# Kernel optimization log

Hardware: AMD Instinct MI355X
Metric: run time of the kernel (lower is better)

The kernel has to match this reference:

```python
import jax, jax.numpy as jnp
import numpy as np

B, T, E, H = 2, 4096, 1024, 16
SEGS = (256, 512, 1024, 2048, 4096)
DILS = (1, 2, 4, 8, 16)
NEG = -1e8  # torchscale uses -1e8 for uncovered / masked lse entries


def setup_inputs() -> dict:
    key = jax.random.key(0)
    ks = jax.random.split(key, 5)
    sc = 0.02
    zb = jnp.zeros((E,), jnp.float32)
    return {
        "x": jax.random.normal(ks[0], (B, T, E), jnp.float32),
        "wq": jax.random.normal(ks[1], (E, E), jnp.float32) * sc,
        "bq": zb,
        "wk": jax.random.normal(ks[2], (E, E), jnp.float32) * sc,
        "bk": zb,
        "wv": jax.random.normal(ks[3], (E, E), jnp.float32) * sc,
        "bv": zb,
        "wo": jax.random.normal(ks[4], (E, E), jnp.float32) * sc,
        "bo": zb,
    }


def _scale_attn(q, k, v, w, r):
    # One LongNet scale: segment length w, dilation ratio r.
    # Head group g = head // (H//r) attends to in-segment positions p with p % r == g
    # (torchscale dense_to_sparse diagonal over (r1, r2)).
    Bq, Tq, Hq, d = q.shape
    n, s, hp = Tq // w, w // r, Hq // r  # segments, sparse length, heads per group

    def gather(x):
        # [B,T,H,d] -> segments [B,n,w,H,d]; split w=(s,r1) (p=l*r+r1) and H=(r2,hp);
        # keep diagonal r1 == r2.
        x = x.reshape(Bq, n, s, r, r, hp, d)
        x = jnp.diagonal(x, axis1=3, axis2=4)          # [B,n,s,hp,d,r]
        return jnp.moveaxis(x, -1, 3).reshape(Bq, n, s, Hq, d)

    qs, ks_, vs = gather(q), gather(k), gather(v)
    scores = jnp.einsum('bnqhd,bnkhd->bnhqk', qs, ks_)
    mask = jnp.tril(jnp.ones((s, s), dtype=bool))       # causal within sparse segment
    scores = jnp.where(mask, scores, NEG)
    lse = jax.scipy.special.logsumexp(scores, axis=-1)  # [B,n,h,q]
    out = jnp.einsum('bnhqk,bnkhd->bnqhd', jax.nn.softmax(scores, axis=-1), vs)

    # Scatter back to dense positions (sparse_to_dense): uncovered -> out 0, lse -1e8.
    eye = jnp.eye(r, dtype=out.dtype)
    out_g = out.reshape(Bq, n, s, r, hp, d)                               # heads as (g, hp)
    dense = jnp.einsum('bnsghd,pg->bnspghd', out_g, eye).reshape(Bq, Tq, Hq, d)
    lse_g = jnp.transpose(lse, (0, 1, 3, 2)).reshape(Bq, n, s, r, hp)     # [B,n,s,g,hp]
    lse_d = jnp.where(eye[:, :, None] > 0, lse_g[:, :, :, None, :, :], NEG)
    return dense, lse_d.reshape(Bq, Tq, Hq)


def reference(x, wq, bq, wk, bk, wv, bv, wo, bo):
    d = E // H
    q = (x @ wq + bq).reshape(B, T, H, d) * (d ** -0.5)
    k = (x @ wk + bk).reshape(B, T, H, d)
    v = (x @ wv + bv).reshape(B, T, H, d)
    outs, lses = [], []
    for w_, r_ in zip(SEGS, DILS):
        o, l = _scale_attn(q, k, v, w_, r_)
        outs.append(o)
        lses.append(l)
    # Merge scales with softmax over per-scale log-sum-exp (dense-attention equivalence).
    wgt = jax.nn.softmax(jnp.stack(lses), axis=0)[..., None]  # [S,B,T,H,1]
    y = jnp.sum(jnp.stack(outs) * wgt, axis=0).reshape(B, T, E)
    return y @ wo + bo
```

## Files before the change

### kernel.cpp

```cpp
#include <hip/hip_runtime.h>
#include <hip/hip_bf16.h>

typedef __bf16 bf16_t;
typedef __bf16 bf16x8 __attribute__((ext_vector_type(8)));
typedef __bf16 bf16x4 __attribute__((ext_vector_type(4)));
typedef float f32x4 __attribute__((ext_vector_type(4)));
typedef int vint4 __attribute__((ext_vector_type(4)));

#define AS1 __attribute__((address_space(1)))
#define AS3 __attribute__((address_space(3)))

constexpr int B_ = 2, T_ = 4096, E_ = 1024, H_ = 16;
constexpr int M_ = B_ * T_;

__device__ constexpr size_t OB_OFF[5]  = {0, 8388608, 12582912, 14680064, 15728640};
__device__ constexpr size_t LSE_OFF[5] = {0, 131072, 196608, 229376, 245760};
constexpr size_t OB_TOTAL  = 16252928;
constexpr size_t LSE_TOTAL = 253952;

__global__ __launch_bounds__(256) void cvt_f32_bf16(const float* __restrict__ in,
                                                    bf16_t* __restrict__ out) {
  int i = (blockIdx.x * 256 + threadIdx.x) * 4;
  const float4 v = *(const float4*)(in + i);
  bf16x4 o;
  o[0] = (bf16_t)v.x; o[1] = (bf16_t)v.y; o[2] = (bf16_t)v.z; o[3] = (bf16_t)v.w;
  *(bf16x4*)(out + i) = o;
}

__global__ __launch_bounds__(256) void cvt_transpose_w(
    const float* __restrict__ w0, const float* __restrict__ w1,
    const float* __restrict__ w2, const float* __restrict__ w3,
    bf16_t* __restrict__ o0, bf16_t* __restrict__ o1,
    bf16_t* __restrict__ o2, bf16_t* __restrict__ o3) {
  __shared__ float tile[32][33];
  const float* src; bf16_t* dst;
  switch (blockIdx.z) {
    case 0: src = w0; dst = o0; break;
    case 1: src = w1; dst = o1; break;
    case 2: src = w2; dst = o2; break;
    default: src = w3; dst = o3; break;
  }
  const int n0 = blockIdx.x * 32, k0 = blockIdx.y * 32;
  const int tx = threadIdx.x & 31, ty = threadIdx.x >> 5;
#pragma unroll
  for (int i = 0; i < 32; i += 8)
    tile[ty + i][tx] = src[(size_t)(k0 + ty + i) * E_ + n0 + tx];
  __syncthreads();
#pragma unroll
  for (int i = 0; i < 32; i += 8)
    dst[(size_t)(n0 + ty + i) * E_ + k0 + tx] = (bf16_t)tile[tx][ty + i];
}

template <bool OUT_BF16, bool QKV>
__global__ __launch_bounds__(256, 4) void gemm_bt(
    const bf16_t* __restrict__ A, const bf16_t* __restrict__ BT,
    const float* __restrict__ bias0, const float* __restrict__ bias1,
    const float* __restrict__ bias2, void* __restrict__ Cout, float qscale) {
  constexpr int K = E_;
  __shared__ bf16_t As[128 * 64];
  __shared__ bf16_t Bs[128 * 64];
  const int tid = threadIdx.x;
  const int lane = tid & 63;
  const int wave = tid >> 6;
  const int wm = wave >> 1, wn = wave & 1;
  const int lc = lane & 15, lg = lane >> 4;
  const int bm = blockIdx.x;
  int bn = blockIdx.y;

  const float* bias = bias0;
  float scale = 1.0f;
  void* outp = Cout;
  const bf16_t* Bt = BT;
  if (QKV) {
    const int which = bn >> 3;
    bn &= 7;
    bias = (which == 0) ? bias0 : (which == 1) ? bias1 : bias2;
    scale = (which == 0) ? qscale : 1.0f;
    outp = (void*)((bf16_t*)Cout + (size_t)which * M_ * E_);
    Bt += (size_t)which * E_ * E_;
  }

  f32x4 acc[4][4] = {};

  const int lrow = tid >> 3;
  const int schunk = (tid & 7) ^ (lrow & 7);
  const bf16_t* Ag = A + (size_t)(bm * 128 + lrow) * K + schunk * 8;
  const bf16_t* Bg = Bt + (size_t)(bn * 128 + lrow) * K + schunk * 8;

  const int sl0 = ((0 * 4 + lg) ^ (lc & 7)) * 8;
  const int sl1 = ((1 * 4 + lg) ^ (lc & 7)) * 8;

  for (int k0 = 0; k0 < K; k0 += 64) {
    __syncthreads();
#pragma unroll
    for (int p = 0; p < 4; ++p) {
      __builtin_amdgcn_global_load_lds(
          (const AS1 void*)(Ag + (size_t)(p * 32) * K + k0),
          (AS3 void*)(As + p * 2048 + tid * 8), 16, 0, 0);
      __builtin_amdgcn_global_load_lds(
          (const AS1 void*)(Bg + (size_t)(p * 32) * K + k0),
          (AS3 void*)(Bs + p * 2048 + tid * 8), 16, 0, 0);
    }
    __syncthreads();
#pragma unroll
    for (int kk = 0; kk < 2; ++kk) {
      const int sl = kk ? sl1 : sl0;
      bf16x8 af[4], bfr[4];
#pragma unroll
      for (int i = 0; i < 4; ++i) {
        af[i]  = *(const bf16x8*)&As[(wm * 64 + i * 16 + lc) * 64 + sl];
        bfr[i] = *(const bf16x8*)&Bs[(wn * 64 + i * 16 + lc) * 64 + sl];
      }
#pragma unroll
      for (int i = 0; i < 4; ++i)
#pragma unroll
        for (int j = 0; j < 4; ++j)
          acc[i][j] = __builtin_amdgcn_mfma_f32_16x16x32_bf16(af[i], bfr[j], acc[i][j], 0, 0, 0);
    }
  }

#pragma unroll
  for (int i = 0; i < 4; ++i) {
    const int row = bm * 128 + wm * 64 + i * 16 + lg * 4;
#pragma unroll
    for (int j = 0; j < 4; ++j) {
      const int col = bn * 128 + wn * 64 + j * 16 + lc;
      const float bv = bias[col];
#pragma unroll
      for (int rg = 0; rg < 4; ++rg) {
        const float v = (acc[i][j][rg] + bv) * scale;
        if (OUT_BF16)
          ((bf16_t*)outp)[(size_t)(row + rg) * E_ + col] = (bf16_t)v;
        else
          ((float*)outp)[(size_t)(row + rg) * E_ + col] = v;
      }
    }
  }
}

template <bool S0>
__global__ __launch_bounds__(512, 4) void attn_inst(
    const bf16_t* __restrict__ Q, const bf16_t* __restrict__ K,
    const bf16_t* __restrict__ V, bf16_t* __restrict__ Ob,
    float* __restrict__ Lse, bf16_t* __restrict__ Y) {
  __shared__ alignas(16) bf16_t Ks[256][72];
  __shared__ alignas(16) bf16_t Vt[64][264];
  __shared__ alignas(16) bf16_t Pw[8][16][40];

  const int bid = blockIdx.x;
  int s, ibase;
  if (S0) { s = 0; ibase = 0; }
  else if (bid < 256) { s = 1; ibase = 0; }
  else if (bid < 384) { s = 2; ibase = 256; }
  else if (bid < 448) { s = 3; ibase = 384; }
  else                { s = 4; ibase = 448; }
  const int inst = bid - ibase;
  const int h = inst & 15;
  const int nseg_log = 4 - s;
  const int seg = (inst >> 4) & ((1 << nseg_log) - 1);
  const int b = inst >> (4 + nseg_log);
  const int g = h >> (4 - s);

  const int t = threadIdx.x;
  const int lane = t & 63;
  const int wv = t >> 6;
  const int lc = lane & 15;
  const int lg = lane >> 4;

  {
    const int row = t >> 1, ch = (t & 1) * 32;
    const int tk = ((seg * 256 + row) << s) + g;
    const size_t off = ((size_t)b * T_ + tk) * E_ + h * 64 + ch;
    const bf16_t* Kg = K + off;
    const bf16_t* Vg = V + off;
#pragma unroll
    for (int j = 0; j < 4; ++j)
      *(bf16x8*)&Ks[row][ch + j * 8] = *(const bf16x8*)(Kg + j * 8);
#pragma unroll
    for (int j = 0; j < 4; ++j) {
      bf16x8 va = *(const bf16x8*)(Vg + j * 8);
#pragma unroll
      for (int e = 0; e < 8; ++e) Vt[ch + j * 8 + e][row] = va[e];
    }
  }
  __syncthreads();

  const size_t rowbase = (size_t)(b * H_ + h) * (T_ >> s) + seg * 256;

#pragma unroll
  for (int sel = 0; sel < 2; ++sel) {
    const int tile = sel ? (15 - wv) : wv;
    const int q = tile * 16 + lc;

    const int tq = ((seg * 256 + q) << s) + g;
    const bf16_t* Qg = Q + ((size_t)b * T_ + tq) * E_ + h * 64 + lg * 8;
    bf16x8 qfrag0 = *(const bf16x8*)(Qg);
    bf16x8 qfrag1 = *(const bf16x8*)(Qg + 32);

    float m = -INFINITY, Z = 0.0f;
    f32x4 Oa[4] = {};

    const int nkb = tile / 4 + 1;
    const int diag = tile / 4;
    for (int kb = 0; kb < nkb; ++kb) {
      f32x4 sacc[4] = {};
      __builtin_amdgcn_s_setprio(1);
#pragma unroll
      for (int kt = 0; kt < 4; ++kt) {
        bf16x8 kf0 = *(const bf16x8*)&Ks[kb * 64 + kt * 16 + lc][lg * 8];
        bf16x8 kf1 = *(const bf16x8*)&Ks[kb * 64 + kt * 16 + lc][32 + lg * 8];
        sacc[kt] = __builtin_amdgcn_mfma_f32_16x16x32_bf16(kf0, qfrag0, sacc[kt], 0, 0, 0);
        sacc[kt] = __builtin_amdgcn_mfma_f32_16x16x32_bf16(kf1, qfrag1, sacc[kt], 0, 0, 0);
      }
      __builtin_amdgcn_s_setprio(0);
      if (kb == diag) {
#pragma unroll
        for (int kt = 0; kt < 4; ++kt)
#pragma unroll
          for (int rg = 0; rg < 4; ++rg)
            if (kb * 64 + kt * 16 + lg * 4 + rg > q) sacc[kt][rg] = -1e30f;
      }
      float pm = -1e30f;
#pragma unroll
      for (int kt = 0; kt < 4; ++kt) {
        pm = fmaxf(pm, fmaxf(fmaxf(sacc[kt][0], sacc[kt][1]),
                             fmaxf(sacc[kt][2], sacc[kt][3])));
      }
      pm = fmaxf(pm, __shfl_xor(pm, 16));
      pm = fmaxf(pm, __shfl_xor(pm, 32));
      if (!__all(pm - m <= 11.5f)) {
        const float nm = fmaxf(m, pm);
        const float crr = __builtin_amdgcn_exp2f(m - nm);
        Z *= crr;
#pragma unroll
        for (int dt = 0; dt < 4; ++dt)
#pragma unroll
          for (int rg = 0; rg < 4; ++rg) Oa[dt][rg] *= crr;
        m = nm;
      }
      float psum = 0.0f;
      bf16x4 pv[4];
#pragma unroll
      for (int kt = 0; kt < 4; ++kt)
#pragma unroll
        for (int rg = 0; rg < 4; ++rg) {
          const float p = __builtin_amdgcn_exp2f(sacc[kt][rg] - m);
          psum += p;
          pv[kt][rg] = (bf16_t)p;
        }
      psum += __shfl_xor(psum, 16);
      psum += __shfl_xor(psum, 32);
      Z += psum;
#pragma unroll
      for (int hf = 0; hf < 2; ++hf) {
        *(bf16x4*)&Pw[wv][lc][lg * 4]      = pv[hf * 2 + 0];
        *(bf16x4*)&Pw[wv][lc][16 + lg * 4] = pv[hf * 2 + 1];
        bf16x8 pb = *(const bf16x8*)&Pw[wv][lc][lg * 8];
        __builtin_amdgcn_s_setprio(1);
#pragma unroll
        for (int dt = 0; dt < 4; ++dt) {
          bf16x8 vf = *(const bf16x8*)&Vt[dt * 16 + lc][(kb * 2 + hf) * 32 + lg * 8];
          Oa[dt] = __builtin_amdgcn_mfma_f32_16x16x32_bf16(vf, pb, Oa[dt], 0, 0, 0);
        }
        __builtin_amdgcn_s_setprio(0);
      }
    }

    const float lse = m + __builtin_amdgcn_logf(Z);
    const float iZ = 1.0f / Z;
    if (!S0) {
      bf16_t* orow = Ob + OB_OFF[s] + (rowbase + q) * 64 + lg * 4;
#pragma unroll
      for (int dt = 0; dt < 4; ++dt) {
        bf16x4 ov;
        ov[0] = (bf16_t)(Oa[dt][0] * iZ);
        ov[1] = (bf16_t)(Oa[dt][1] * iZ);
        ov[2] = (bf16_t)(Oa[dt][2] * iZ);
        ov[3] = (bf16_t)(Oa[dt][3] * iZ);
        *(bf16x4*)(orow + dt * 16) = ov;
      }
      if (lg == 0) Lse[LSE_OFF[s] + rowbase + q] = lse;
    } else {
      const int t_glob = seg * 256 + q;
      float o16[4][4];
#pragma unroll
      for (int dt = 0; dt < 4; ++dt)
#pragma unroll
        for (int rg = 0; rg < 4; ++rg) o16[dt][rg] = Oa[dt][rg] * iZ;
      float M = lse, S = 1.0f;
#pragma unroll
      for (int s2 = 1; s2 <= 4; ++s2) {
        const int r = 1 << s2;
        const int gg = h >> (4 - s2);
        if ((t_glob & (r - 1)) != gg) continue;
        const size_t idx = (size_t)(b * H_ + h) * (T_ >> s2) + (t_glob >> s2);
        const float l2 = Lse[LSE_OFF[s2] + idx];
        const bf16_t* orow = Ob + OB_OFF[s2] + idx * 64 + lg * 4;
        const float nM = fmaxf(M, l2);
        const float a = __builtin_amdgcn_exp2f(M - nM);
        const float e = __builtin_amdgcn_exp2f(l2 - nM);
#pragma unroll
        for (int dt = 0; dt < 4; ++dt) {
          const bf16x4 ov = *(const bf16x4*)(orow + dt * 16);
#pragma unroll
          for (int rg = 0; rg < 4; ++rg)
            o16[dt][rg] = o16[dt][rg] * a + (float)ov[rg] * e;
        }
        S = S * a + e;
        M = nM;
      }
      const float invS = 1.0f / S;
      bf16_t* yrow = Y + ((size_t)b * T_ + t_glob) * E_ + h * 64 + lg * 4;
#pragma unroll
      for (int dt = 0; dt < 4; ++dt) {
        bf16x4 ov;
        ov[0] = (bf16_t)(o16[dt][0] * invS);
        ov[1] = (bf16_t)(o16[dt][1] * invS);
        ov[2] = (bf16_t)(o16[dt][2] * invS);
        ov[3] = (bf16_t)(o16[dt][3] * invS);
        *(bf16x4*)(yrow + dt * 16) = ov;
      }
    }
  }
}

extern "C" void kernel_launch(void* const* d_in, const int* in_sizes, int n_in,
                              void* d_out, int out_size, void* d_ws, size_t ws_size,
                              hipStream_t stream) {
  (void)in_sizes; (void)n_in; (void)out_size; (void)ws_size;
  const float* x  = (const float*)d_in[0];
  const float* wq = (const float*)d_in[1];
  const float* bq = (const float*)d_in[2];
  const float* wk = (const float*)d_in[3];
  const float* bk = (const float*)d_in[4];
  const float* wv = (const float*)d_in[5];
  const float* bv = (const float*)d_in[6];
  const float* wo = (const float*)d_in[7];
  const float* bo = (const float*)d_in[8];

  char* p = (char*)d_ws;
  auto take = [&](size_t bytes) {
    char* q = p;
    p += (bytes + 255) & ~(size_t)255;
    return (void*)q;
  };
  bf16_t* wq_t = (bf16_t*)take((size_t)E_ * E_ * 2);
  bf16_t* wk_t = (bf16_t*)take((size_t)E_ * E_ * 2);
  bf16_t* wv_t = (bf16_t*)take((size_t)E_ * E_ * 2);
  bf16_t* wo_t = (bf16_t*)take((size_t)E_ * E_ * 2);
  bf16_t* xb   = (bf16_t*)take((size_t)M_ * E_ * 2);
  bf16_t* qb   = (bf16_t*)take((size_t)M_ * E_ * 2);
  bf16_t* kbuf = (bf16_t*)take((size_t)M_ * E_ * 2);
  bf16_t* vbuf = (bf16_t*)take((size_t)M_ * E_ * 2);
  bf16_t* yb   = (bf16_t*)take((size_t)M_ * E_ * 2);
  bf16_t* Ob   = (bf16_t*)take(OB_TOTAL * 2);
  float*  Lse  = (float*)take(LSE_TOTAL * 4);
  (void)wk_t; (void)wv_t;

  cvt_f32_bf16<<<M_ * E_ / 1024, 256, 0, stream>>>(x, xb);
  cvt_transpose_w<<<dim3(32, 32, 4), 256, 0, stream>>>(wq, wk, wv, wo, wq_t, wk_t, wv_t, wo_t);

  gemm_bt<true, true><<<dim3(M_ / 128, 24), 256, 0, stream>>>(
      xb, wq_t, bq, bk, bv, qb, 0.125f * 1.44269504f);

  attn_inst<false><<<480, 512, 0, stream>>>(qb, kbuf, vbuf, Ob, Lse, yb);
  attn_inst<true><<<512, 512, 0, stream>>>(qb, kbuf, vbuf, Ob, Lse, yb);

  gemm_bt<false, false><<<dim3(M_ / 128, 8), 256, 0, stream>>>(
      yb, wo_t, bo, bo, bo, d_out, 1.0f);
}
```

Measured before the change: 126.4 us.

## Swizzle K/V shared layouts, use global_load_lds for K, prefetch merge inputs

Replaces the padded K and transposed-V shared arrays with unpadded XOR-swizzled layouts, and loads K straight into LDS with global_load_lds instead of going through registers. The V transpose now writes bf16x4 chunks instead of single elements, which cuts LDS store instructions. The scale-merge epilogue issues all four cross-scale Lse/Ob loads before the merge loop and turns the skip into predication, so load latency overlaps. The cost is loading data for uncovered scales unconditionally, including indices that may be unused.

```diff
diff --git a/kernel.cpp b/kernel.cpp
--- a/kernel.cpp
+++ b/kernel.cpp
@@ -143,8 +143,8 @@
     const bf16_t* __restrict__ Q, const bf16_t* __restrict__ K,
     const bf16_t* __restrict__ V, bf16_t* __restrict__ Ob,
     float* __restrict__ Lse, bf16_t* __restrict__ Y) {
-  __shared__ alignas(16) bf16_t Ks[256][72];
-  __shared__ alignas(16) bf16_t Vt[64][264];
+  __shared__ alignas(16) bf16_t Ks[256 * 64];
+  __shared__ alignas(16) bf16_t Vt[64 * 256];
   __shared__ alignas(16) bf16_t Pw[8][16][40];
 
   const int bid = blockIdx.x;
@@ -168,19 +168,30 @@
   const int lg = lane >> 4;
 
   {
-    const int row = t >> 1, ch = (t & 1) * 32;
-    const int tk = ((seg * 256 + row) << s) + g;
-    const size_t off = ((size_t)b * T_ + tk) * E_ + h * 64 + ch;
-    const bf16_t* Kg = K + off;
-    const bf16_t* Vg = V + off;
-#pragma unroll
-    for (int j = 0; j < 4; ++j)
-      *(bf16x8*)&Ks[row][ch + j * 8] = *(const bf16x8*)(Kg + j * 8);
-#pragma unroll
-    for (int j = 0; j < 4; ++j) {
-      bf16x8 va = *(const bf16x8*)(Vg + j * 8);
-#pragma unroll
-      for (int e = 0; e < 8; ++e) Vt[ch + j * 8 + e][row] = va[e];
+    const int krow = t >> 3;
+    const int kch = ((t & 7) ^ (krow & 7)) * 8;
+#pragma unroll
+    for (int p = 0; p < 4; ++p) {
+      const int tk = ((seg * 256 + krow + p * 64) << s) + g;
+      __builtin_amdgcn_global_load_lds(
+          (const AS1 void*)(K + ((size_t)b * T_ + tk) * E_ + h * 64 + kch),
+          (AS3 void*)(Ks + p * 4096 + t * 8), 16, 0, 0);
+    }
+  }
+  {
+    const int r0 = (t & 63) * 4;
+    const int d0 = (t >> 6) * 8;
+    bf16x8 va[4];
+#pragma unroll
+    for (int rr = 0; rr < 4; ++rr) {
+      const int tk = ((seg * 256 + r0 + rr) << s) + g;
+      va[rr] = *(const bf16x8*)(V + ((size_t)b * T_ + tk) * E_ + h * 64 + d0);
+    }
+#pragma unroll
+    for (int d = 0; d < 8; ++d) {
+      bf16x4 w;
+      w[0] = va[0][d]; w[1] = va[1][d]; w[2] = va[2][d]; w[3] = va[3][d];
+      *(bf16x4*)&Vt[(d0 + d) * 256 + (r0 ^ ((d & 7) << 3))] = w;
     }
   }
   __syncthreads();
@@ -202,13 +213,15 @@
 
     const int nkb = tile / 4 + 1;
     const int diag = tile / 4;
+    const int kxor = (lc & 7);
     for (int kb = 0; kb < nkb; ++kb) {
       f32x4 sacc[4] = {};
       __builtin_amdgcn_s_setprio(1);
 #pragma unroll
       for (int kt = 0; kt < 4; ++kt) {
-        bf16x8 kf0 = *(const bf16x8*)&Ks[kb * 64 + kt * 16 + lc][lg * 8];
-        bf16x8 kf1 = *(const bf16x8*)&Ks[kb * 64 + kt * 16 + lc][32 + lg * 8];
+        const int krow = kb * 64 + kt * 16 + lc;
+        bf16x8 kf0 = *(const bf16x8*)&Ks[krow * 64 + ((0 + lg) ^ kxor) * 8];
+        bf16x8 kf1 = *(const bf16x8*)&Ks[krow * 64 + ((4 + lg) ^ kxor) * 8];
         sacc[kt] = __builtin_amdgcn_mfma_f32_16x16x32_bf16(kf0, qfrag0, sacc[kt], 0, 0, 0);
         sacc[kt] = __builtin_amdgcn_mfma_f32_16x16x32_bf16(kf1, qfrag1, sacc[kt], 0, 0, 0);
       }
@@ -259,7 +272,9 @@
         __builtin_amdgcn_s_setprio(1);
 #pragma unroll
         for (int dt = 0; dt < 4; ++dt) {
-          bf16x8 vf = *(const bf16x8*)&Vt[dt * 16 + lc][(kb * 2 + hf) * 32 + lg * 8];
+          const int vrow = dt * 16 + lc;
+          const int vcol = ((kb * 2 + hf) * 32 + lg * 8) ^ ((lc & 7) << 3);
+          bf16x8 vf = *(const bf16x8*)&Vt[vrow * 256 + vcol];
           Oa[dt] = __builtin_amdgcn_mfma_f32_16x16x32_bf16(vf, pb, Oa[dt], 0, 0, 0);
         }
         __builtin_amdgcn_s_setprio(0);
@@ -282,6 +297,17 @@
       if (lg == 0) Lse[LSE_OFF[s] + rowbase + q] = lse;
     } else {
       const int t_glob = seg * 256 + q;
+      float l2v[4];
+      bf16x4 ovv[4][4];
+#pragma unroll
+      for (int s2 = 1; s2 <= 4; ++s2) {
+        const size_t idx = (size_t)(b * H_ + h) * (T_ >> s2) + (t_glob >> s2);
+        l2v[s2 - 1] = Lse[LSE_OFF[s2] + idx];
+        const bf16_t* orow = Ob + OB_OFF[s2] + idx * 64 + lg * 4;
+#pragma unroll
+        for (int dt = 0; dt < 4; ++dt)
+          ovv[s2 - 1][dt] = *(const bf16x4*)(orow + dt * 16);
+      }
       float o16[4][4];
 #pragma unroll
       for (int dt = 0; dt < 4; ++dt)
@@ -292,20 +318,16 @@
       for (int s2 = 1; s2 <= 4; ++s2) {
         const int r = 1 << s2;
         const int gg = h >> (4 - s2);
-        if ((t_glob & (r - 1)) != gg) continue;
-        const size_t idx = (size_t)(b * H_ + h) * (T_ >> s2) + (t_glob >> s2);
-        const float l2 = Lse[LSE_OFF[s2] + idx];
-        const bf16_t* orow = Ob + OB_OFF[s2] + idx * 64 + lg * 4;
+        const bool cov = ((t_glob & (r - 1)) == gg);
+        const float l2 = cov ? l2v[s2 - 1] : -INFINITY;
         const float nM = fmaxf(M, l2);
         const float a = __builtin_amdgcn_exp2f(M - nM);
         const float e = __builtin_amdgcn_exp2f(l2 - nM);
 #pragma unroll
-        for (int dt = 0; dt < 4; ++dt) {
-          const bf16x4 ov = *(const bf16x4*)(orow + dt * 16);
+        for (int dt = 0; dt < 4; ++dt)
 #pragma unroll
           for (int rg = 0; rg < 4; ++rg)
-            o16[dt][rg] = o16[dt][rg] * a + (float)ov[rg] * e;
-        }
+            o16[dt][rg] = o16[dt][rg] * a + (float)ovv[s2 - 1][dt][rg] * e;
         S = S * a + e;
         M = nM;
       }
```

Result: no change. 127.9 us (+1.2%).
